# Kernel optimization log

Hardware: AMD Instinct MI355X
Metric: run time of the kernel (lower is better)

The kernel has to match this reference:

```python
import jax, jax.numpy as jnp
import numpy as np

# SoftMoE dims: batch B, tokens M, token dim D, experts E, slots P, expert hidden F
B, M, D, E, P, F = 4, 1024, 768, 16, 64, 3072  # P = ceil(M*num_outputs*capacity/E) = 64


def setup_inputs() -> dict:
    key = jax.random.key(0)
    k0, k1, k2, k3 = jax.random.split(key, 4)
    x = jax.random.normal(k0, (B, M, D), jnp.float32)
    # lecun_normal: std = 1/sqrt(fan_in)
    phi = jax.random.normal(k1, (D, E, P), jnp.float32) / np.sqrt(D).astype(np.float32)
    # per-expert 2-layer MLP params (vmap variable_axes={'params':0} -> leading expert axis)
    W1 = jax.random.normal(k2, (E, D, F), jnp.float32) / np.sqrt(D).astype(np.float32)
    b1 = jnp.zeros((E, F), jnp.float32)
    W2 = jax.random.normal(k3, (E, F, D), jnp.float32) / np.sqrt(F).astype(np.float32)
    b2 = jnp.zeros((E, D), jnp.float32)
    return {"x": x, "phi": phi, "W1": W1, "b1": b1, "W2": W2, "b2": b2}


def reference(x, phi, W1, b1, W2, b2):
    # routing logits: [B, M, E, P]
    logits = jnp.einsum('bmd,dnp->bmnp', x, phi)
    # dispatch: softmax over tokens (axis=1)
    dispatch = jax.nn.softmax(logits, axis=1)
    # combine: joint softmax over (experts, slots)
    b_, m_, e_, p_ = logits.shape
    combine = jax.nn.softmax(logits.reshape(b_, m_, e_ * p_), axis=-1).reshape(b_, m_, e_, p_)
    # dispatch tokens into expert slots: [B, E, P, D]
    mix = jnp.nan_to_num(jnp.einsum('bmd,bmnp->bnpd', x, dispatch))
    # per-expert MLP (grouped GEMM over expert axis n), returns (out, hidden)
    hidden = jax.nn.gelu(jnp.einsum('bnpd,ndf->bnpf', mix, W1) + b1[None, :, None, :])
    expert_out = jnp.einsum('bnpf,nfd->bnpd', hidden, W2) + b2[None, :, None, :]
    # combine expert slot outputs back to tokens: [B, M, D]
    outputs = jnp.einsum('bnpd,bmnp->bmd', expert_out, combine)
    probabilities = combine.mean(axis=-1)                      # [B, M, E]
    top_experts = jnp.argmax(probabilities, axis=2, keepdims=True)  # [B, M, 1]
    return outputs, probabilities, top_experts, hidden
```

## Files before the change

### kernel.cpp

```cpp
#include <hip/hip_runtime.h>
#include <hip/hip_bf16.h>


typedef unsigned short u16;
typedef __bf16 bf16x8 __attribute__((ext_vector_type(8)));
typedef float f32x4 __attribute__((ext_vector_type(4)));

__device__ __forceinline__ float gelu_f(float x) {
    const float c = 0.7978845608028654f;
    float u = c * (x + 0.044715f * x * x * x);
    return 0.5f * x * (1.0f + tanhf(u));
}

__device__ __forceinline__ u16 f2b(float x) {
    union { float f; unsigned u; } v; v.f = x;
    unsigned r = v.u + 0x7FFF + ((v.u >> 16) & 1);
    return (u16)(r >> 16);
}

template<bool TRANSA, bool DOGELU>
__global__ __launch_bounds__(256)
void gemm_k(const float* __restrict__ A, const float* __restrict__ Bm,
            const float* __restrict__ bias, float* __restrict__ C,
            int K, int lda, int ldb, int ldc,
            long aZ, long bZ, long cZ, int biasZ,
            long rgsA, long rgsC)
{
    __shared__ float As[16][128];
    __shared__ float Bs[16][64];
    const int z = blockIdx.z;
    A  += (long)z * aZ;
    Bm += (long)z * bZ;
    if (bias) bias += (long)z * biasZ;
    const int row0 = blockIdx.y * 128;
    const int col0 = blockIdx.x * 64;
    const int t  = threadIdx.x;
    const int tx = t & 15;
    const int ty = t >> 4;

    float acc[8][4];
    #pragma unroll
    for (int i = 0; i < 8; ++i)
        #pragma unroll
        for (int j = 0; j < 4; ++j) acc[i][j] = 0.f;

    for (int k0 = 0; k0 < K; k0 += 16) {
        if (TRANSA) {
            const int kk = t >> 5;
            const int ii = (t & 31) * 4;
            const float* pa = A + (long)(k0 + kk) * lda + (row0 + ii);
            float4 v0 = *(const float4*)pa;
            float4 v1 = *(const float4*)(pa + 8L * lda);
            *(float4*)&As[kk][ii]     = v0;
            *(float4*)&As[kk + 8][ii] = v1;
        } else {
            const int ii = t >> 1;
            const int kk = (t & 1) * 8;
            const int grow = row0 + ii;
            const float* pa = A + (long)(grow >> 6) * rgsA
                                + (long)(grow & 63) * lda + (k0 + kk);
            float4 v0 = *(const float4*)pa;
            float4 v1 = *(const float4*)(pa + 4);
            As[kk+0][ii] = v0.x; As[kk+1][ii] = v0.y;
            As[kk+2][ii] = v0.z; As[kk+3][ii] = v0.w;
            As[kk+4][ii] = v1.x; As[kk+5][ii] = v1.y;
            As[kk+6][ii] = v1.z; As[kk+7][ii] = v1.w;
        }
        {
            const int kk = t >> 4;
            const int jj = (t & 15) * 4;
            float4 v = *(const float4*)(Bm + (long)(k0 + kk) * ldb + (col0 + jj));
            *(float4*)&Bs[kk][jj] = v;
        }
        __syncthreads();
        #pragma unroll
        for (int k = 0; k < 16; ++k) {
            float a[8], b[4];
            *(float4*)&a[0] = *(const float4*)&As[k][ty * 8];
            *(float4*)&a[4] = *(const float4*)&As[k][ty * 8 + 4];
            *(float4*)&b[0] = *(const float4*)&Bs[k][tx * 4];
            #pragma unroll
            for (int i = 0; i < 8; ++i)
                #pragma unroll
                for (int j = 0; j < 4; ++j)
                    acc[i][j] = fmaf(a[i], b[j], acc[i][j]);
        }
        __syncthreads();
    }

    float bj[4] = {0.f, 0.f, 0.f, 0.f};
    if (bias) {
        #pragma unroll
        for (int j = 0; j < 4; ++j) bj[j] = bias[col0 + tx * 4 + j];
    }
    #pragma unroll
    for (int i = 0; i < 8; ++i) {
        const int grow = row0 + ty * 8 + i;
        const long rb = (long)(grow >> 6) * rgsC
                      + (long)(grow & 63) * ldc + (col0 + tx * 4);
        float rv[4];
        #pragma unroll
        for (int j = 0; j < 4; ++j) {
            float v = acc[i][j] + bj[j];
            if (DOGELU) v = gelu_f(v);
            rv[j] = v;
        }
        *(float4*)(C + (long)z * cZ + rb) = make_float4(rv[0], rv[1], rv[2], rv[3]);
    }
}

template<bool AF32, bool DOGELU, bool CF32>
__global__ __launch_bounds__(256)
void mfma_gemm(const void* __restrict__ Av, const u16* __restrict__ Bt,
               const float* __restrict__ bias, void* __restrict__ Cv,
               int K, int lda, int ldb, int ldc,
               long aZ, long bZ, long cZ, int biasZ,
               long rgsA, long rgsC, int nbx, int nblk)
{
    __shared__ u16 As[128][64];
    __shared__ u16 Bs[128][64];
    const int flat = blockIdx.x;
    const int nper = gridDim.x >> 3;
    const int r    = (flat & 7) * nper + (flat >> 3);
    const int z    = r / nblk;
    const int bi   = r - z * nblk;
    const int by   = bi / nbx;
    const int bx   = bi - by * nbx;

    const int row0 = by * 128;
    const int col0 = bx * 128;
    const int t    = threadIdx.x;
    const int lane = t & 63;
    const int wave = t >> 6;
    const int wr   = (wave >> 1) * 64;
    const int wc   = (wave & 1) * 64;

    const int srow  = t >> 1;
    const int shalf = t & 1;
    const int agrow = row0 + srow;
    const long aRowOff = (long)z * aZ + (long)(agrow >> 6) * rgsA
                       + (long)(agrow & 63) * lda;
    const long bRowOff = (long)z * bZ + (long)(col0 + srow) * ldb;

    f32x4 acc[4][4] = {};

    for (int k0 = 0; k0 < K; k0 += 64) {
        if (AF32) {
            const float* pa = (const float*)Av + aRowOff + k0 + shalf * 32;
            #pragma unroll
            for (int q = 0; q < 4; ++q) {
                float4 u0 = *(const float4*)(pa + q * 8);
                float4 u1 = *(const float4*)(pa + q * 8 + 4);
                u16 tmp[8] = { f2b(u0.x), f2b(u0.y), f2b(u0.z), f2b(u0.w),
                               f2b(u1.x), f2b(u1.y), f2b(u1.z), f2b(u1.w) };
                const int cs = (shalf * 4 + q) ^ (srow & 7);
                *(uint4*)&As[srow][cs * 8] = *(const uint4*)tmp;
            }
        } else {
            const u16* pa = (const u16*)Av + aRowOff + k0 + shalf * 32;
            #pragma unroll
            for (int q = 0; q < 4; ++q) {
                uint4 v = *(const uint4*)(pa + q * 8);
                const int cs = (shalf * 4 + q) ^ (srow & 7);
                *(uint4*)&As[srow][cs * 8] = v;
            }
        }
        {
            const u16* pb = Bt + bRowOff + k0 + shalf * 32;
            #pragma unroll
            for (int q = 0; q < 4; ++q) {
                uint4 v = *(const uint4*)(pb + q * 8);
                const int cs = (shalf * 4 + q) ^ (srow & 7);
                *(uint4*)&Bs[srow][cs * 8] = v;
            }
        }
        __syncthreads();

        #pragma unroll
        for (int kk = 0; kk < 2; ++kk) {
            const int cchunk = kk * 4 + (lane >> 4);
            bf16x8 af[4], bfr[4];
            #pragma unroll
            for (int i = 0; i < 4; ++i) {
                const int m = wr + i * 16 + (lane & 15);
                af[i]  = __builtin_bit_cast(bf16x8,
                           *(const uint4*)&As[m][(cchunk ^ (m & 7)) * 8]);
                const int n = wc + i * 16 + (lane & 15);
                bfr[i] = __builtin_bit_cast(bf16x8,
                           *(const uint4*)&Bs[n][(cchunk ^ (n & 7)) * 8]);
            }
            #pragma unroll
            for (int i = 0; i < 4; ++i)
                #pragma unroll
                for (int j = 0; j < 4; ++j)
                    acc[i][j] = __builtin_amdgcn_mfma_f32_16x16x32_bf16(
                                    af[i], bfr[j], acc[i][j], 0, 0, 0);
        }
        __syncthreads();
    }

    const int cq = lane >> 4;
    #pragma unroll
    for (int j = 0; j < 4; ++j) {
        const int gcol = col0 + wc + j * 16 + (lane & 15);
        const float bv = bias ? bias[(long)z * biasZ + gcol] : 0.f;
        #pragma unroll
        for (int i = 0; i < 4; ++i) {
            #pragma unroll
            for (int r2 = 0; r2 < 4; ++r2) {
                const int grow = row0 + wr + i * 16 + cq * 4 + r2;
                const long co = (long)z * cZ + (long)(grow >> 6) * rgsC
                              + (long)(grow & 63) * ldc + gcol;
                float v = acc[i][j][r2] + bv;
                if (DOGELU) v = gelu_f(v);
                if (CF32) ((float*)Cv)[co] = v;
                else      ((u16*)Cv)[co]  = f2b(v);
            }
        }
    }
}

__global__ __launch_bounds__(256)
void f32_to_b16(const float* __restrict__ in, u16* __restrict__ out)
{
    const long i = ((long)blockIdx.x * 256 + threadIdx.x) * 8;
    float4 a = *(const float4*)(in + i);
    float4 b = *(const float4*)(in + i + 4);
    u16 tmp[8] = { f2b(a.x), f2b(a.y), f2b(a.z), f2b(a.w),
                   f2b(b.x), f2b(b.y), f2b(b.z), f2b(b.w) };
    *(uint4*)(out + i) = *(const uint4*)tmp;
}

template<bool F32>
__global__ __launch_bounds__(256)
void transpose_k(const void* __restrict__ inV, u16* __restrict__ out, int R, int C)
{
    __shared__ u16 tile[64][72];
    const long zin = (long)blockIdx.z * R * C;
    const int r0 = blockIdx.y * 64, c0 = blockIdx.x * 64;
    const int t  = threadIdx.x;
    const int tr = t >> 4;
    const int tc = (t & 15) * 4;
    #pragma unroll
    for (int p = 0; p < 4; ++p) {
        const int r = tr + p * 16;
        if (F32) {
            float4 v = *(const float4*)((const float*)inV + zin + (long)(r0 + r) * C + c0 + tc);
            tile[r][tc+0] = f2b(v.x); tile[r][tc+1] = f2b(v.y);
            tile[r][tc+2] = f2b(v.z); tile[r][tc+3] = f2b(v.w);
        } else {
            ushort4 v = *(const ushort4*)((const u16*)inV + zin + (long)(r0 + r) * C + c0 + tc);
            tile[r][tc+0] = v.x; tile[r][tc+1] = v.y;
            tile[r][tc+2] = v.z; tile[r][tc+3] = v.w;
        }
    }
    __syncthreads();
    #pragma unroll
    for (int p = 0; p < 4; ++p) {
        const int rr = tr + p * 16;
        ushort4 o;
        o.x = tile[tc+0][rr]; o.y = tile[tc+1][rr];
        o.z = tile[tc+2][rr]; o.w = tile[tc+3][rr];
        *(ushort4*)(out + (long)blockIdx.z * R * C + (long)(c0 + rr) * R + r0 + tc) = o;
    }
}

__global__ __launch_bounds__(1024)
void softmax_m(float* __restrict__ logits)
{
    const int b   = blockIdx.y;
    const int c   = threadIdx.x & 15;
    const int col = blockIdx.x * 16 + c;
    const int mg  = threadIdx.x >> 4;
    float* base = logits + (long)b * 1048576 + col;

    float vals[16];
    float mx = -3.4e38f;
    #pragma unroll
    for (int i = 0; i < 16; ++i) {
        float v = base[(long)(mg * 16 + i) * 1024];
        vals[i] = v;
        mx = fmaxf(mx, v);
    }
    __shared__ float red[64][16];
    red[mg][c] = mx;
    __syncthreads();
    for (int s = 32; s >= 1; s >>= 1) {
        if (mg < s) red[mg][c] = fmaxf(red[mg][c], red[mg + s][c]);
        __syncthreads();
    }
    mx = red[0][c];
    __syncthreads();
    float ssum = 0.f;
    #pragma unroll
    for (int i = 0; i < 16; ++i) { vals[i] = expf(vals[i] - mx); ssum += vals[i]; }
    red[mg][c] = ssum;
    __syncthreads();
    for (int s = 32; s >= 1; s >>= 1) {
        if (mg < s) red[mg][c] += red[mg + s][c];
        __syncthreads();
    }
    const float inv = 1.f / red[0][c];
    #pragma unroll
    for (int i = 0; i < 16; ++i)
        base[(long)(mg * 16 + i) * 1024] = vals[i] * inv;
}

__global__ __launch_bounds__(1024)
void softmax_mT(const float* __restrict__ logits, u16* __restrict__ dispT)
{
    const int b   = blockIdx.y;
    const int c   = threadIdx.x & 15;
    const int col = blockIdx.x * 16 + c;
    const int mg  = threadIdx.x >> 4;
    const float* base = logits + (long)b * 1048576 + col;

    float vals[16];
    float mx = -3.4e38f;
    #pragma unroll
    for (int i = 0; i < 16; ++i) {
        float v = base[(long)(mg * 16 + i) * 1024];
        vals[i] = v;
        mx = fmaxf(mx, v);
    }
    __shared__ float red[64][16];
    red[mg][c] = mx;
    __syncthreads();
    for (int s = 32; s >= 1; s >>= 1) {
        if (mg < s) red[mg][c] = fmaxf(red[mg][c], red[mg + s][c]);
        __syncthreads();
    }
    mx = red[0][c];
    __syncthreads();
    float ssum = 0.f;
    #pragma unroll
    for (int i = 0; i < 16; ++i) { vals[i] = expf(vals[i] - mx); ssum += vals[i]; }
    red[mg][c] = ssum;
    __syncthreads();
    for (int s = 32; s >= 1; s >>= 1) {
        if (mg < s) red[mg][c] += red[mg + s][c];
        __syncthreads();
    }
    const float inv = 1.f / red[0][c];

    union { u16 s[16]; uint4 q[2]; } pk;
    #pragma unroll
    for (int i = 0; i < 16; ++i) pk.s[i] = f2b(vals[i] * inv);
    u16* ob = dispT + (long)b * 1048576 + (long)col * 1024 + mg * 16;
    *(uint4*)ob       = pk.q[0];
    *(uint4*)(ob + 8) = pk.q[1];
}

template<bool B16>
__global__ __launch_bounds__(256)
void softmax_ep(const float* __restrict__ logits, void* __restrict__ comb,
                float* __restrict__ probs, float* __restrict__ tops)
{
    const long r = blockIdx.x;
    const int  t = threadIdx.x;
    const float* row = logits + r * 1024;
    float4 v = *(const float4*)(row + t * 4);

    float mx = fmaxf(fmaxf(v.x, v.y), fmaxf(v.z, v.w));
    #pragma unroll
    for (int s = 32; s; s >>= 1) mx = fmaxf(mx, __shfl_xor(mx, s));
    __shared__ float wr_[4];
    const int wid = t >> 6;
    if ((t & 63) == 0) wr_[wid] = mx;
    __syncthreads();
    mx = fmaxf(fmaxf(wr_[0], wr_[1]), fmaxf(wr_[2], wr_[3]));
    __syncthreads();

    float e0 = expf(v.x - mx), e1 = expf(v.y - mx);
    float e2 = expf(v.z - mx), e3 = expf(v.w - mx);
    float s4 = e0 + e1 + e2 + e3;
    float sm = s4;
    #pragma unroll
    for (int s = 32; s; s >>= 1) sm += __shfl_xor(sm, s);
    if ((t & 63) == 0) wr_[wid] = sm;
    __syncthreads();
    const float tot = wr_[0] + wr_[1] + wr_[2] + wr_[3];
    const float inv = 1.f / tot;

    if (B16) {
        ushort4 o;
        o.x = f2b(e0 * inv); o.y = f2b(e1 * inv);
        o.z = f2b(e2 * inv); o.w = f2b(e3 * inv);
        *(ushort4*)((u16*)comb + r * 1024 + t * 4) = o;
    } else {
        float4 o = make_float4(e0 * inv, e1 * inv, e2 * inv, e3 * inv);
        *(float4*)((float*)comb + r * 1024 + t * 4) = o;
    }

    __shared__ float es[16][16];
    es[t >> 4][t & 15] = s4 * inv;
    __syncthreads();
    __shared__ float pr[16];
    if (t < 16) {
        float ss = 0.f;
        #pragma unroll
        for (int i = 0; i < 16; ++i) ss += es[t][i];
        float p = ss * (1.f / 64.f);
        probs[r * 16 + t] = p;
        pr[t] = p;
    }
    __syncthreads();
    if (t == 0) {
        int best = 0; float bv = pr[0];
        #pragma unroll
        for (int e = 1; e < 16; ++e)
            if (pr[e] > bv) { bv = pr[e]; best = e; }
        tops[r] = (float)best;
    }
}

extern "C" void kernel_launch(void* const* d_in, const int* in_sizes, int n_in,
                              void* d_out, int out_size, void* d_ws, size_t ws_size,
                              hipStream_t stream)
{
    (void)in_sizes; (void)n_in; (void)out_size;
    const float* x   = (const float*)d_in[0];
    const float* phi = (const float*)d_in[1];
    const float* W1  = (const float*)d_in[2];
    const float* b1  = (const float*)d_in[3];
    const float* W2  = (const float*)d_in[4];
    const float* b2  = (const float*)d_in[5];

    float* outputs = (float*)d_out;
    float* probs   = outputs + 3145728;
    float* tops    = outputs + 3145728 + 65536;
    float* hid     = outputs + 3145728 + 65536 + 4096;

    char* wsb = (char*)d_ws;

    if (ws_size >= 209715200ull) {
        float* logits = (float*)(wsb);
        u16*   combB  = (u16*)(wsb + 16777216);
        u16*   dispT  = (u16*)(wsb + 25165824);
        u16*   xT     = (u16*)(wsb + 33554432);
        u16*   mixB   = (u16*)(wsb + 39845888);
        u16*   W1T    = (u16*)(wsb + 46137344);
        u16*   W2T    = (u16*)(wsb + 121634816);
        u16*   eoutN  = (u16*)(wsb + 197132288);
        u16*   eoutT  = (u16*)(wsb + 203423744);
        u16*   hidB   = W1T;

        transpose_k<true><<<dim3(48, 12, 16), 256, 0, stream>>>(W1, W1T, 768, 3072);
        transpose_k<true><<<dim3(12, 48, 16), 256, 0, stream>>>(W2, W2T, 3072, 768);
        transpose_k<true><<<dim3(12, 16, 4),  256, 0, stream>>>(x,  xT,  1024, 768);

        gemm_k<false, false><<<dim3(16, 32, 1), 256, 0, stream>>>(
            x, phi, nullptr, logits,
            768, 768, 1024, 1024, 0L, 0L, 0L, 0, 64L * 768, 64L * 1024);

        softmax_ep<true><<<dim3(4096), 256, 0, stream>>>(logits, combB, probs, tops);
        softmax_mT<<<dim3(64, 4), 1024, 0, stream>>>(logits, dispT);

        mfma_gemm<false, false, false><<<dim3(192), 256, 0, stream>>>(
            dispT, xT, nullptr, mixB,
            1024, 1024, 1024, 768, 1048576L, 786432L, 786432L, 0,
            65536L, 49152L, 6, 48);

        mfma_gemm<false, true, true><<<dim3(768), 256, 0, stream>>>(
            mixB, W1T, b1, hid,
            768, 768, 768, 3072, 49152L, 2359296L, 196608L, 3072,
            786432L, 3145728L, 24, 48);

        f32_to_b16<<<dim3(6144), 256, 0, stream>>>(hid, hidB);

        mfma_gemm<false, false, false><<<dim3(192), 256, 0, stream>>>(
            hidB, W2T, b2, eoutN,
            3072, 3072, 3072, 768, 196608L, 2359296L, 49152L, 768,
            3145728L, 786432L, 6, 12);

        transpose_k<false><<<dim3(12, 16, 4), 256, 0, stream>>>(eoutN, eoutT, 1024, 768);

        mfma_gemm<false, false, true><<<dim3(192), 256, 0, stream>>>(
            combB, eoutT, nullptr, outputs,
            1024, 1024, 1024, 768, 1048576L, 786432L, 786432L, 0,
            65536L, 49152L, 6, 48);
    } else {
        float* logits = (float*)wsb;
        float* comb   = (float*)(wsb + 16777216);
        float* mixb   = (float*)(wsb + 33554432);
        float* eout   = (float*)wsb;

        gemm_k<false, false><<<dim3(16, 32, 1), 256, 0, stream>>>(
            x, phi, nullptr, logits,
            768, 768, 1024, 1024, 0L, 0L, 0L, 0, 64L * 768, 64L * 1024);
        softmax_ep<false><<<dim3(4096), 256, 0, stream>>>(logits, comb, probs, tops);
        softmax_m<<<dim3(64, 4), 1024, 0, stream>>>(logits);
        gemm_k<true, false><<<dim3(12, 8, 4), 256, 0, stream>>>(
            logits, x, nullptr, mixb,
            1024, 1024, 768, 768, 1048576L, 786432L, 786432L, 0, 0L, 64L * 768);
        gemm_k<false, true><<<dim3(48, 2, 16), 256, 0, stream>>>(
            mixb, W1, b1, hid,
            768, 768, 3072, 3072, 49152L, 2359296L, 196608L, 3072,
            786432L, 3145728L);
        gemm_k<false, false><<<dim3(12, 2, 16), 256, 0, stream>>>(
            hid, W2, b2, eout,
            3072, 3072, 768, 768, 196608L, 2359296L, 49152L, 768,
            3145728L, 786432L);
        gemm_k<false, false><<<dim3(12, 8, 4), 256, 0, stream>>>(
            comb, eout, nullptr, outputs,
            1024, 1024, 768, 768, 1048576L, 786432L, 786432L, 0,
            64L * 1024, 64L * 768);
    }
}
```

Before: 660.5 us.

## Fuse bf16 hidden conversion into W1 GEMM epilogue and add tiled logits GEMM

The W1 GEMM epilogue now writes a bf16 copy of the GELU hidden activations straight into workspace (offset 0). This removes the separate f32_to_b16 pass that re-read the 50 MB fp32 hidden tensor. The hidden bf16 buffer moves from the W1T region to the workspace start, which overlaps logits and combB; those appear to be consumed before the write, but that should be checked. The logits GEMM is also replaced by a dedicated 512-thread, 128x128-tile, double-buffered fp32 kernel with register prefetch.

```diff
diff --git a/kernel.cpp b/kernel.cpp
--- a/kernel.cpp
+++ b/kernel.cpp
@@ -16,6 +16,80 @@
     union { float f; unsigned u; } v; v.f = x;
     unsigned r = v.u + 0x7FFF + ((v.u >> 16) & 1);
     return (u16)(r >> 16);
+}
+
+__global__ __launch_bounds__(512)
+void gemm_logits(const float* __restrict__ x, const float* __restrict__ phi,
+                 float* __restrict__ C)
+{
+    __shared__ float As[2][16][132];
+    __shared__ float Bs[2][16][128];
+    const int col0 = blockIdx.x * 128;
+    const int row0 = blockIdx.y * 128;
+    const int t = threadIdx.x;
+
+    const int arow = t >> 2, akk = (t & 3) * 4;
+    const int bkk  = t >> 5, bcc = (t & 31) * 4;
+    const float* pa = x   + (long)(row0 + arow) * 768 + akk;
+    const float* pb = phi + (long)bkk * 1024 + col0 + bcc;
+
+    const int ty = t >> 4, tx = t & 15;
+
+    float acc[4][8];
+    #pragma unroll
+    for (int i = 0; i < 4; ++i)
+        #pragma unroll
+        for (int j = 0; j < 8; ++j) acc[i][j] = 0.f;
+
+    float4 ra = *(const float4*)pa;
+    float4 rb = *(const float4*)pb;
+    As[0][akk+0][arow] = ra.x;
+    As[0][akk+1][arow] = ra.y;
+    As[0][akk+2][arow] = ra.z;
+    As[0][akk+3][arow] = ra.w;
+    *(float4*)&Bs[0][bkk][bcc] = rb;
+
+    int cur = 0;
+    for (int kt = 0; kt < 48; ++kt) {
+        if (kt + 1 < 48) {
+            ra = *(const float4*)(pa + (kt + 1) * 16);
+            rb = *(const float4*)(pb + (long)(kt + 1) * 16 * 1024);
+        }
+        __syncthreads();
+        #pragma unroll
+        for (int k = 0; k < 16; ++k) {
+            float a[4], bl[4], bh[4];
+            *(float4*)a  = *(const float4*)&As[cur][k][ty * 4];
+            *(float4*)bl = *(const float4*)&Bs[cur][k][tx * 4];
+            *(float4*)bh = *(const float4*)&Bs[cur][k][64 + tx * 4];
+            #pragma unroll
+            for (int i = 0; i < 4; ++i) {
+                #pragma unroll
+                for (int j = 0; j < 4; ++j) {
+                    acc[i][j]     = fmaf(a[i], bl[j], acc[i][j]);
+                    acc[i][j + 4] = fmaf(a[i], bh[j], acc[i][j + 4]);
+                }
+            }
+        }
+        if (kt + 1 < 48) {
+            const int nxt = cur ^ 1;
+            As[nxt][akk+0][arow] = ra.x;
+            As[nxt][akk+1][arow] = ra.y;
+            As[nxt][akk+2][arow] = ra.z;
+            As[nxt][akk+3][arow] = ra.w;
+            *(float4*)&Bs[nxt][bkk][bcc] = rb;
+            cur = nxt;
+        }
+    }
+
+    #pragma unroll
+    for (int i = 0; i < 4; ++i) {
+        const long ro = (long)(row0 + ty * 4 + i) * 1024 + col0;
+        *(float4*)&C[ro + tx * 4] =
+            make_float4(acc[i][0], acc[i][1], acc[i][2], acc[i][3]);
+        *(float4*)&C[ro + 64 + tx * 4] =
+            make_float4(acc[i][4], acc[i][5], acc[i][6], acc[i][7]);
+    }
 }
 
 template<bool TRANSA, bool DOGELU>
@@ -113,6 +187,7 @@
 __global__ __launch_bounds__(256)
 void mfma_gemm(const void* __restrict__ Av, const u16* __restrict__ Bt,
                const float* __restrict__ bias, void* __restrict__ Cv,
+               u16* __restrict__ Cb2,
                int K, int lda, int ldb, int ldc,
                long aZ, long bZ, long cZ, int biasZ,
                long rgsA, long rgsC, int nbx, int nblk)
@@ -215,20 +290,10 @@
                 if (DOGELU) v = gelu_f(v);
                 if (CF32) ((float*)Cv)[co] = v;
                 else      ((u16*)Cv)[co]  = f2b(v);
+                if (Cb2)  Cb2[co] = f2b(v);
             }
         }
     }
-}
-
-__global__ __launch_bounds__(256)
-void f32_to_b16(const float* __restrict__ in, u16* __restrict__ out)
-{
-    const long i = ((long)blockIdx.x * 256 + threadIdx.x) * 8;
-    float4 a = *(const float4*)(in + i);
-    float4 b = *(const float4*)(in + i + 4);
-    u16 tmp[8] = { f2b(a.x), f2b(a.y), f2b(a.z), f2b(a.w),
-                   f2b(b.x), f2b(b.y), f2b(b.z), f2b(b.w) };
-    *(uint4*)(out + i) = *(const uint4*)tmp;
 }
 
 template<bool F32>
@@ -443,40 +508,36 @@
         u16*   W2T    = (u16*)(wsb + 121634816);
         u16*   eoutN  = (u16*)(wsb + 197132288);
         u16*   eoutT  = (u16*)(wsb + 203423744);
-        u16*   hidB   = W1T;
+        u16*   hidB   = (u16*)wsb;
 
         transpose_k<true><<<dim3(48, 12, 16), 256, 0, stream>>>(W1, W1T, 768, 3072);
         transpose_k<true><<<dim3(12, 48, 16), 256, 0, stream>>>(W2, W2T, 3072, 768);
         transpose_k<true><<<dim3(12, 16, 4),  256, 0, stream>>>(x,  xT,  1024, 768);
 
-        gemm_k<false, false><<<dim3(16, 32, 1), 256, 0, stream>>>(
-            x, phi, nullptr, logits,
-            768, 768, 1024, 1024, 0L, 0L, 0L, 0, 64L * 768, 64L * 1024);
+        gemm_logits<<<dim3(8, 32), 512, 0, stream>>>(x, phi, logits);
 
         softmax_ep<true><<<dim3(4096), 256, 0, stream>>>(logits, combB, probs, tops);
         softmax_mT<<<dim3(64, 4), 1024, 0, stream>>>(logits, dispT);
 
         mfma_gemm<false, false, false><<<dim3(192), 256, 0, stream>>>(
-            dispT, xT, nullptr, mixB,
+            dispT, xT, nullptr, mixB, nullptr,
             1024, 1024, 1024, 768, 1048576L, 786432L, 786432L, 0,
             65536L, 49152L, 6, 48);
 
         mfma_gemm<false, true, true><<<dim3(768), 256, 0, stream>>>(
-            mixB, W1T, b1, hid,
+            mixB, W1T, b1, hid, hidB,
             768, 768, 768, 3072, 49152L, 2359296L, 196608L, 3072,
             786432L, 3145728L, 24, 48);
 
-        f32_to_b16<<<dim3(6144), 256, 0, stream>>>(hid, hidB);
-
         mfma_gemm<false, false, false><<<dim3(192), 256, 0, stream>>>(
-            hidB, W2T, b2, eoutN,
+            hidB, W2T, b2, eoutN, nullptr,
             3072, 3072, 3072, 768, 196608L, 2359296L, 49152L, 768,
             3145728L, 786432L, 6, 12);
 
         transpose_k<false><<<dim3(12, 16, 4), 256, 0, stream>>>(eoutN, eoutT, 1024, 768);
 
         mfma_gemm<false, false, true><<<dim3(192), 256, 0, stream>>>(
-            combB, eoutT, nullptr, outputs,
+            combB, eoutT, nullptr, outputs, nullptr,
             1024, 1024, 1024, 768, 1048576L, 786432L, 786432L, 0,
             65536L, 49152L, 6, 48);
     } else {
```

After: 649.8 us. About the same (-1.6%).
